# Kernel tuning notes

Measured on AMD Instinct MI355X. Metric: run time of the kernel, lower is better.

The kernel has to match this reference:

```python
import jax, jax.numpy as jnp
import numpy as np

HIDDEN = 512
NUM_EXPERTS = 8


def moe_top1(h, gate_w, We, be):
    # h: [B,S,d]; gate_w: [d,E]; We: [E,d,d]; be: [E,d]
    logits = jnp.einsum('bsd,de->bse', h, gate_w)
    probs = jax.nn.softmax(logits, axis=-1)            # [B,S,E]
    idx = jnp.argmax(probs, axis=-1)                   # [B,S] top-1 expert
    top_p = jnp.max(probs, axis=-1)                    # [B,S] gate weight
    # dense per-expert outputs then one-hot select (reference form of dispatch/combine)
    y_all = jnp.einsum('bsd,edf->bsef', h, We) + be    # [B,S,E,d]
    onehot = jax.nn.one_hot(idx, NUM_EXPERTS, dtype=h.dtype)
    out = jnp.einsum('bse,bsef->bsf', onehot, y_all)
    return out * top_p[..., None]


def setup_inputs() -> dict:
    key = jax.random.key(0)
    ks = jax.random.split(key, 10)
    B, S, d, E = 8, 2048, HIDDEN, NUM_EXPERTS
    s = 1.0 / np.sqrt(d)
    return {
        'x':   jax.random.normal(ks[0], (B, S, d), dtype=jnp.float32),
        'W1':  jax.random.uniform(ks[1], (d, d), jnp.float32, -s, s),
        'b1':  jax.random.uniform(ks[2], (d,), jnp.float32, -s, s),
        'gw2': jax.random.uniform(ks[3], (d, E), jnp.float32, -s, s),
        'We2': jax.random.uniform(ks[4], (E, d, d), jnp.float32, -s, s),
        'be2': jax.random.uniform(ks[5], (E, d), jnp.float32, -s, s),
        'gw3': jax.random.uniform(ks[6], (d, E), jnp.float32, -s, s),
        'We3': jax.random.uniform(ks[7], (E, d, d), jnp.float32, -s, s),
        'be3': jax.random.uniform(ks[8], (E, d), jnp.float32, -s, s),
        'y':   jax.random.randint(ks[9], (B,), 0, d, dtype=jnp.int64 if jax.config.jax_enable_x64 else jnp.int32),
    }


def reference(x, W1, b1, gw2, We2, be2, gw3, We3, be3, y):
    h = jnp.einsum('bsd,fd->bsf', x, W1.T.T @ jnp.eye(W1.shape[0], dtype=W1.dtype)) if False else x @ W1.T + b1  # Linear(d,d)
    out = moe_top1(h, gw2, We2, be2)
    out = moe_top1(out, gw3, We3, be3)
    hidden = h + out
    sentence_embed = hidden.mean(axis=1)               # [B, d]
    logp = jax.nn.log_softmax(sentence_embed, axis=-1)
    loss = -jnp.take_along_axis(logp, y[:, None].astype(jnp.int32), axis=1).mean()
    return loss
```

## Files before the change

kernel.cpp:

```cpp
#include <hip/hip_runtime.h>
#include <cstdint>

#define T_TOK 16384
#define D     512
#define E     8

typedef __attribute__((ext_vector_type(4))) float f32x4;
typedef __attribute__((ext_vector_type(8))) short short8v;
typedef __attribute__((ext_vector_type(8))) unsigned short u16x8;

__device__ __forceinline__ unsigned short f2bf(float f) {
    unsigned u = __float_as_uint(f);
    u += 0x7FFF + ((u >> 16) & 1);
    return (unsigned short)(u >> 16);
}
__device__ __forceinline__ float bf2f(unsigned short h) {
    return __uint_as_float((unsigned)h << 16);
}
__device__ __forceinline__ int swz(int r, int g) {
    return (r << 6) + (((g ^ ((r >> 1) & 3)) & 3) << 4);
}

__global__ __launch_bounds__(256) void k_conv_w1(const float* __restrict__ W,
                                                 unsigned short* __restrict__ hi,
                                                 unsigned short* __restrict__ lo,
                                                 int* __restrict__ c2,
                                                 int* __restrict__ c3,
                                                 float* __restrict__ embed)
{
    const int tid = threadIdx.x;
    if (blockIdx.x == 256) {
        if (tid < E) { c2[tid] = 0; c3[tid] = 0; }
        for (int i = tid; i < 8 * D; i += 256) embed[i] = 0.f;
        return;
    }
    const int i = (blockIdx.x * 256 + tid) * 4;
    const float4 v = *(const float4*)(W + i);
    const float f[4] = {v.x, v.y, v.z, v.w};
    unsigned short h[4], l[4];
#pragma unroll
    for (int j = 0; j < 4; ++j) {
        h[j] = f2bf(f[j]);
        l[j] = f2bf(f[j] - bf2f(h[j]));
    }
    *(uint2*)(hi + i) = *(uint2*)h;
    *(uint2*)(lo + i) = *(uint2*)l;
}

__global__ __launch_bounds__(256) void k_prep_we(const float* __restrict__ We2,
                                                 const float* __restrict__ We3,
                                                 unsigned short* __restrict__ hi2,
                                                 unsigned short* __restrict__ lo2,
                                                 unsigned short* __restrict__ hi3,
                                                 unsigned short* __restrict__ lo3)
{
    __shared__ float t[32][33];
    const int z = blockIdx.z;
    const int e = z & 7;
    const float* src = (z < 8 ? We2 : We3) + ((size_t)e << 18);
    unsigned short* dh = (z < 8 ? hi2 : hi3) + ((size_t)e << 18);
    unsigned short* dl = (z < 8 ? lo2 : lo3) + ((size_t)e << 18);
    const int k0 = blockIdx.x << 5, n0 = blockIdx.y << 5;
    const int tx = threadIdx.x & 31, ty = threadIdx.x >> 5;
#pragma unroll
    for (int i = 0; i < 32; i += 8)
        t[ty + i][tx] = src[(size_t)(k0 + ty + i) * D + n0 + tx];
    __syncthreads();
    const int n  = threadIdx.x >> 3;
    const int kc = (threadIdx.x & 7) << 2;
    unsigned short h4[4], l4[4];
#pragma unroll
    for (int j = 0; j < 4; ++j) {
        const float f = t[kc + j][n];
        h4[j] = f2bf(f);
        l4[j] = f2bf(f - bf2f(h4[j]));
    }
    const size_t o = (size_t)(n0 + n) * D + k0 + kc;
    *(uint2*)(dh + o) = *(uint2*)h4;
    *(uint2*)(dl + o) = *(uint2*)l4;
}

__global__ __launch_bounds__(256) void k_gating(const float* __restrict__ H,
                                                const float* __restrict__ gw,
                                                float* __restrict__ p,
                                                int* __restrict__ lists,
                                                int* __restrict__ counts)
{
    __shared__ float gws[D * E];
    __shared__ int histo[E], basex[E];
    const int tid = threadIdx.x;
    for (int i = tid; i < D * E; i += 256) gws[i] = gw[i];
    if (tid < E) histo[tid] = 0;
    __syncthreads();

    const int part = tid & 7;
    const int slot = tid >> 3;
    const int t0 = (blockIdx.x << 6) + slot;
    const int t1 = t0 + 32;
    const int d0 = part << 6;

    float a0[E], a1[E];
#pragma unroll
    for (int e = 0; e < E; ++e) { a0[e] = 0.f; a1[e] = 0.f; }
    const float* h0 = H + (size_t)t0 * D + d0;
    const float* h1 = H + (size_t)t1 * D + d0;
#pragma unroll 4
    for (int i = 0; i < 64; i += 4) {
        const float4 v0 = *(const float4*)(h0 + i);
        const float4 v1 = *(const float4*)(h1 + i);
        const float* gp = gws + (size_t)(d0 + i) * E;
#pragma unroll
        for (int j = 0; j < 4; ++j) {
            const f32x4 gA = *(const f32x4*)(gp + j * E);
            const f32x4 gB = *(const f32x4*)(gp + j * E + 4);
            const float x0 = (j == 0) ? v0.x : (j == 1) ? v0.y : (j == 2) ? v0.z : v0.w;
            const float x1 = (j == 0) ? v1.x : (j == 1) ? v1.y : (j == 2) ? v1.z : v1.w;
#pragma unroll
            for (int e = 0; e < 4; ++e) {
                a0[e]     += x0 * gA[e];
                a0[e + 4] += x0 * gB[e];
                a1[e]     += x1 * gA[e];
                a1[e + 4] += x1 * gB[e];
            }
        }
    }
#pragma unroll
    for (int e = 0; e < E; ++e) {
#pragma unroll
        for (int o = 1; o < 8; o <<= 1) {
            a0[e] += __shfl_xor(a0[e], o, 8);
            a1[e] += __shfl_xor(a1[e], o, 8);
        }
    }

    int mi0 = 0, mi1 = 0, r0 = 0, r1 = 0;
    if (part == 0) {
        float m0 = a0[0], m1 = a1[0];
#pragma unroll
        for (int e = 1; e < E; ++e) {
            if (a0[e] > m0) { m0 = a0[e]; mi0 = e; }
            if (a1[e] > m1) { m1 = a1[e]; mi1 = e; }
        }
        float s0 = 0.f, s1 = 0.f;
#pragma unroll
        for (int e = 0; e < E; ++e) { s0 += expf(a0[e] - m0); s1 += expf(a1[e] - m1); }
        p[t0] = 1.0f / s0;
        p[t1] = 1.0f / s1;
        r0 = atomicAdd(&histo[mi0], 1);
        r1 = atomicAdd(&histo[mi1], 1);
    }
    __syncthreads();
    if (tid < E) basex[tid] = atomicAdd(&counts[tid], histo[tid]);
    __syncthreads();
    if (part == 0) {
        lists[mi0 * T_TOK + basex[mi0] + r0] = t0;
        lists[mi1 * T_TOK + basex[mi1] + r1] = t1;
    }
}

template <bool GATHER>
__global__ __launch_bounds__(256, 2) void k_gemm_mfma(
    const float* __restrict__ A,
    const unsigned short* __restrict__ Bh,
    const unsigned short* __restrict__ Bl,
    const float* __restrict__ bias,
    const float* __restrict__ scale,
    const int* __restrict__ lists,
    const int* __restrict__ counts,
    float* __restrict__ C)
{
    __shared__ __align__(16) char sAh[8192];
    __shared__ __align__(16) char sAl[8192];
    __shared__ __align__(16) char sBh[8192];
    __shared__ __align__(16) char sBl[8192];
    __shared__ int Ts[128];

    const int tid = threadIdx.x;
    const int cpx = gridDim.x >> 3;
    const int wg  = (blockIdx.x & 7) * cpx + (blockIdx.x >> 3);
    const int mt  = wg >> 2;
    const int n0  = (wg & 3) << 7;

    int listoff = 0, mcnt = 128;
    size_t boff = 0;
    const float* bb = bias;
    if constexpr (GATHER) {
        int acc8 = 0, eSel = -1, mstart = 0;
#pragma unroll
        for (int i = 0; i < 8; ++i) {
            const int c = counts[i];
            const int nt = (c + 127) >> 7;
            if (eSel < 0 && mt < acc8 + nt) { eSel = i; mstart = (mt - acc8) << 7; }
            acc8 += nt;
        }
        if (eSel < 0) return;
        mcnt = min(128, counts[eSel] - mstart);
        listoff = eSel * T_TOK + mstart;
        boff = (size_t)eSel << 18;
        bb = bias + (eSel << 9);
    }

    if (tid < 128) {
        int t;
        if constexpr (GATHER) t = (tid < mcnt) ? lists[listoff + tid] : -1;
        else                  t = (mt << 7) + tid;
        Ts[tid] = t;
    }
    __syncthreads();

    const int srow = tid >> 1;
    const int sk   = (tid & 1) << 4;
    const int tA   = Ts[srow];
    const float* ap = A + (size_t)(tA < 0 ? 0 : tA) * D + sk;
    const unsigned short* bph = Bh + boff + (size_t)(n0 + srow) * D + sk;
    const unsigned short* bpl = Bl + boff + (size_t)(n0 + srow) * D + sk;
    const int g0  = sk >> 3;
    const int wa0 = swz(srow, g0), wa1 = swz(srow, g0 + 1);

    float4 av0 = *(const float4*)ap,        av1 = *(const float4*)(ap + 4),
           av2 = *(const float4*)(ap + 8),  av3 = *(const float4*)(ap + 12);
    uint4 bh0 = *(const uint4*)bph, bh1 = *(const uint4*)(bph + 8);
    uint4 bl0 = *(const uint4*)bpl, bl1 = *(const uint4*)(bpl + 8);

    const int wid = tid >> 6, lane = tid & 63;
    const int wr = (wid >> 1) << 6;
    const int wc = (wid & 1) << 6;
    const int fr = lane & 15;
    const int fg = lane >> 4;

    f32x4 acc[4][4] = {};

#pragma unroll 1
    for (int kt = 0; kt < 16; ++kt) {
        u16x8 h0, h1, l0, l1;
        {
            float f[16];
            *(float4*)&f[0] = av0; *(float4*)&f[4]  = av1;
            *(float4*)&f[8] = av2; *(float4*)&f[12] = av3;
#pragma unroll
            for (int i = 0; i < 8; ++i) {
                const unsigned short hh = f2bf(f[i]);
                h0[i] = hh;
                l0[i] = f2bf(f[i] - bf2f(hh));
            }
#pragma unroll
            for (int i = 0; i < 8; ++i) {
                const unsigned short hh = f2bf(f[8 + i]);
                h1[i] = hh;
                l1[i] = f2bf(f[8 + i] - bf2f(hh));
            }
        }
        __syncthreads();
        *(u16x8*)(sAh + wa0) = h0;  *(u16x8*)(sAh + wa1) = h1;
        *(u16x8*)(sAl + wa0) = l0;  *(u16x8*)(sAl + wa1) = l1;
        *(uint4*)(sBh + wa0) = bh0; *(uint4*)(sBh + wa1) = bh1;
        *(uint4*)(sBl + wa0) = bl0; *(uint4*)(sBl + wa1) = bl1;
        __syncthreads();
        if (kt < 15) {
            ap += 32; bph += 32; bpl += 32;
            av0 = *(const float4*)ap;       av1 = *(const float4*)(ap + 4);
            av2 = *(const float4*)(ap + 8); av3 = *(const float4*)(ap + 12);
            bh0 = *(const uint4*)bph; bh1 = *(const uint4*)(bph + 8);
            bl0 = *(const uint4*)bpl; bl1 = *(const uint4*)(bpl + 8);
        }

        short8v a_h[4], a_l[4], b_h[4], b_l[4];
#pragma unroll
        for (int i = 0; i < 4; ++i) {
            const int r = wr + i * 16 + fr;
            a_h[i] = *(const short8v*)(sAh + swz(r, fg));
            a_l[i] = *(const short8v*)(sAl + swz(r, fg));
        }
#pragma unroll
        for (int j = 0; j < 4; ++j) {
            const int r = wc + j * 16 + fr;
            b_h[j] = *(const short8v*)(sBh + swz(r, fg));
            b_l[j] = *(const short8v*)(sBl + swz(r, fg));
        }
#pragma unroll
        for (int i = 0; i < 4; ++i)
#pragma unroll
            for (int j = 0; j < 4; ++j) {
                acc[i][j] = __builtin_amdgcn_mfma_f32_16x16x32_bf16(a_h[i], b_h[j], acc[i][j], 0, 0, 0);
                acc[i][j] = __builtin_amdgcn_mfma_f32_16x16x32_bf16(a_h[i], b_l[j], acc[i][j], 0, 0, 0);
                acc[i][j] = __builtin_amdgcn_mfma_f32_16x16x32_bf16(a_l[i], b_h[j], acc[i][j], 0, 0, 0);
            }
    }

    float bj[4];
#pragma unroll
    for (int j = 0; j < 4; ++j) bj[j] = bb[n0 + wc + j * 16 + fr];
#pragma unroll
    for (int i = 0; i < 4; ++i) {
#pragma unroll
        for (int r = 0; r < 4; ++r) {
            const int m = wr + i * 16 + fg * 4 + r;
            const int t = Ts[m];
            if (t < 0) continue;
            float s = 1.f;
            if constexpr (GATHER) s = scale[t];
            float* cp = C + (size_t)t * D + n0 + wc;
#pragma unroll
            for (int j = 0; j < 4; ++j)
                cp[j * 16 + fr] = (acc[i][j][r] + bj[j]) * s;
        }
    }
}

__global__ __launch_bounds__(256) void k_reduce(const float* __restrict__ H,
                                                const float* __restrict__ O3,
                                                float* __restrict__ embed)
{
    const int b = blockIdx.x;
    const int sc = blockIdx.y;
    const int f = threadIdx.x;
    const size_t base = ((size_t)b * 2048 + (size_t)sc * 32) * D;
    const float* hb = H + base;
    const float* ob = O3 + base;
    float a0 = 0.f, a1 = 0.f;
#pragma unroll 4
    for (int s = 0; s < 32; ++s) {
        a0 += hb[s * D + f]       + ob[s * D + f];
        a1 += hb[s * D + f + 256] + ob[s * D + f + 256];
    }
    atomicAdd(&embed[b * D + f],       a0 * (1.0f / 2048.0f));
    atomicAdd(&embed[b * D + f + 256], a1 * (1.0f / 2048.0f));
}

__global__ __launch_bounds__(512) void k_loss(const float* __restrict__ embed,
                                              const int* __restrict__ y,
                                              float* __restrict__ out)
{
    __shared__ float partial[8];
    const int w = threadIdx.x >> 6;
    const int lane = threadIdx.x & 63;
    const float* row = embed + w * D;

    float v[8];
    float vmax = -1e30f;
#pragma unroll
    for (int i = 0; i < 8; ++i) {
        v[i] = row[lane + i * 64];
        vmax = fmaxf(vmax, v[i]);
    }
#pragma unroll
    for (int o = 32; o > 0; o >>= 1) vmax = fmaxf(vmax, __shfl_xor(vmax, o));
    float s = 0.f;
#pragma unroll
    for (int i = 0; i < 8; ++i) s += expf(v[i] - vmax);
#pragma unroll
    for (int o = 32; o > 0; o >>= 1) s += __shfl_xor(s, o);
    const float lse = vmax + logf(s);
    if (lane == 0) partial[w] = lse - row[y[w]];
    __syncthreads();
    if (threadIdx.x == 0) {
        float l = 0.f;
#pragma unroll
        for (int b = 0; b < 8; ++b) l += partial[b];
        out[0] = l * (1.0f / 8.0f);
    }
}

extern "C" void kernel_launch(void* const* d_in, const int* in_sizes, int n_in,
                              void* d_out, int out_size, void* d_ws, size_t ws_size,
                              hipStream_t stream)
{
    const float* x   = (const float*)d_in[0];
    const float* W1  = (const float*)d_in[1];
    const float* b1  = (const float*)d_in[2];
    const float* gw2 = (const float*)d_in[3];
    const float* We2 = (const float*)d_in[4];
    const float* be2 = (const float*)d_in[5];
    const float* gw3 = (const float*)d_in[6];
    const float* We3 = (const float*)d_in[7];
    const float* be3 = (const float*)d_in[8];
    const int*   y   = (const int*)d_in[9];
    float* out = (float*)d_out;

    char* ws = (char*)d_ws;
    size_t off = 0;
    auto alloc = [&](size_t bytes) -> void* {
        void* p = ws + off;
        off = (off + bytes + 255) & ~(size_t)255;
        return p;
    };
    float* h     = (float*)alloc((size_t)T_TOK * D * 4);
    float* out2  = (float*)alloc((size_t)T_TOK * D * 4);
    float* out3  = (float*)alloc((size_t)T_TOK * D * 4);
    unsigned short* b1h  = (unsigned short*)alloc((size_t)D * D * 2);
    unsigned short* b1l  = (unsigned short*)alloc((size_t)D * D * 2);
    unsigned short* we2h = (unsigned short*)alloc((size_t)E * D * D * 2);
    unsigned short* we2l = (unsigned short*)alloc((size_t)E * D * D * 2);
    unsigned short* we3h = (unsigned short*)alloc((size_t)E * D * D * 2);
    unsigned short* we3l = (unsigned short*)alloc((size_t)E * D * D * 2);
    float* p2    = (float*)alloc((size_t)T_TOK * 4);
    float* p3    = (float*)alloc((size_t)T_TOK * 4);
    int*   l2    = (int*)alloc((size_t)E * T_TOK * 4);
    int*   l3    = (int*)alloc((size_t)E * T_TOK * 4);
    int*   c2    = (int*)alloc(E * 4);
    int*   c3    = (int*)alloc(E * 4);
    float* embed = (float*)alloc(8 * D * 4);
    (void)ws_size; (void)in_sizes; (void)n_in; (void)out_size;

    k_conv_w1<<<dim3(257), dim3(256), 0, stream>>>(W1, b1h, b1l, c2, c3, embed);
    k_prep_we<<<dim3(16, 16, 16), dim3(256), 0, stream>>>(We2, We3, we2h, we2l, we3h, we3l);

    k_gemm_mfma<false><<<dim3(512), dim3(256), 0, stream>>>(
        x, b1h, b1l, b1, nullptr, nullptr, nullptr, h);

    k_gating<<<dim3(256), dim3(256), 0, stream>>>(h, gw2, p2, l2, c2);
    k_gemm_mfma<true><<<dim3(544), dim3(256), 0, stream>>>(
        h, we2h, we2l, be2, p2, l2, c2, out2);

    k_gating<<<dim3(256), dim3(256), 0, stream>>>(out2, gw3, p3, l3, c3);
    k_gemm_mfma<true><<<dim3(544), dim3(256), 0, stream>>>(
        out2, we3h, we3l, be3, p3, l3, c3, out3);

    k_reduce<<<dim3(8, 64), dim3(256), 0, stream>>>(h, out3, embed);
    k_loss<<<dim3(1), dim3(512), 0, stream>>>(embed, y, out);
}
```

Before: 267.8 us.

## Pre-split activations to bf16 hi/lo and stream tiles via global_load_lds

Activations are now split into bf16 hi/lo pairs once: x by a new conversion kernel, and h and out2 inside the GEMM epilogue, which writes extra bf16 copies next to the fp32 output. The GEMM main loop no longer converts fp32 on the fly. It loads all four operand tiles straight from global memory into LDS with global_load_lds, so the register staging and conversion ALU work go away. The cost is extra global writes for the bf16 copies, and the prefetch overlap is lost, because each load is now issued between two barriers within the same iteration. The x copies reuse the out3 buffer, which is safe only because out3 is written later.

```diff
diff --git a/kernel.cpp b/kernel.cpp
--- a/kernel.cpp
+++ b/kernel.cpp
@@ -7,7 +7,6 @@
 
 typedef __attribute__((ext_vector_type(4))) float f32x4;
 typedef __attribute__((ext_vector_type(8))) short short8v;
-typedef __attribute__((ext_vector_type(8))) unsigned short u16x8;
 
 __device__ __forceinline__ unsigned short f2bf(float f) {
     unsigned u = __float_as_uint(f);
@@ -19,6 +18,11 @@
 }
 __device__ __forceinline__ int swz(int r, int g) {
     return (r << 6) + (((g ^ ((r >> 1) & 3)) & 3) << 4);
+}
+__device__ __forceinline__ void gload16(const void* g, void* s) {
+    __builtin_amdgcn_global_load_lds(
+        (const __attribute__((address_space(1))) unsigned int*)g,
+        (__attribute__((address_space(3))) unsigned int*)s, 16, 0, 0);
 }
 
 __global__ __launch_bounds__(256) void k_conv_w1(const float* __restrict__ W,
@@ -45,6 +49,27 @@
     }
     *(uint2*)(hi + i) = *(uint2*)h;
     *(uint2*)(lo + i) = *(uint2*)l;
+}
+
+__global__ __launch_bounds__(256) void k_conv_x(const float* __restrict__ x,
+                                                unsigned short* __restrict__ xh,
+                                                unsigned short* __restrict__ xl)
+{
+    const size_t i = ((size_t)blockIdx.x * 256 + threadIdx.x) * 16;
+    float f[16];
+#pragma unroll
+    for (int q = 0; q < 4; ++q)
+        *(float4*)&f[q * 4] = *(const float4*)(x + i + q * 4);
+    unsigned short h[16], l[16];
+#pragma unroll
+    for (int j = 0; j < 16; ++j) {
+        h[j] = f2bf(f[j]);
+        l[j] = f2bf(f[j] - bf2f(h[j]));
+    }
+    *(uint4*)(xh + i)     = *(uint4*)&h[0];
+    *(uint4*)(xh + i + 8) = *(uint4*)&h[8];
+    *(uint4*)(xl + i)     = *(uint4*)&l[0];
+    *(uint4*)(xl + i + 8) = *(uint4*)&l[8];
 }
 
 __global__ __launch_bounds__(256) void k_prep_we(const float* __restrict__ We2,
@@ -158,16 +183,19 @@
     }
 }
 
-template <bool GATHER>
+template <bool GATHER, bool OUTCONV>
 __global__ __launch_bounds__(256, 2) void k_gemm_mfma(
-    const float* __restrict__ A,
+    const unsigned short* __restrict__ Ah,
+    const unsigned short* __restrict__ Al,
     const unsigned short* __restrict__ Bh,
     const unsigned short* __restrict__ Bl,
     const float* __restrict__ bias,
     const float* __restrict__ scale,
     const int* __restrict__ lists,
     const int* __restrict__ counts,
-    float* __restrict__ C)
+    float* __restrict__ C,
+    unsigned short* __restrict__ Ch,
+    unsigned short* __restrict__ Cl)
 {
     __shared__ __align__(16) char sAh[8192];
     __shared__ __align__(16) char sAl[8192];
@@ -208,21 +236,28 @@
     }
     __syncthreads();
 
-    const int srow = tid >> 1;
-    const int sk   = (tid & 1) << 4;
-    const int tA   = Ts[srow];
-    const float* ap = A + (size_t)(tA < 0 ? 0 : tA) * D + sk;
-    const unsigned short* bph = Bh + boff + (size_t)(n0 + srow) * D + sk;
-    const unsigned short* bpl = Bl + boff + (size_t)(n0 + srow) * D + sk;
-    const int g0  = sk >> 3;
-    const int wa0 = swz(srow, g0), wa1 = swz(srow, g0 + 1);
-
-    float4 av0 = *(const float4*)ap,        av1 = *(const float4*)(ap + 4),
-           av2 = *(const float4*)(ap + 8),  av3 = *(const float4*)(ap + 12);
-    uint4 bh0 = *(const uint4*)bph, bh1 = *(const uint4*)(bph + 8);
-    uint4 bl0 = *(const uint4*)bpl, bl1 = *(const uint4*)(bpl + 8);
-
     const int wid = tid >> 6, lane = tid & 63;
+
+    const int dr  = lane >> 2;
+    const int gsl = lane & 3;
+    const int r0 = (wid << 5) + dr, r1 = r0 + 16;
+    const int gg0 = ((gsl ^ ((r0 >> 1) & 3)) & 3) << 4;
+    const int gg1 = ((gsl ^ ((r1 >> 1) & 3)) & 3) << 4;
+    const int tA0 = Ts[r0] < 0 ? 0 : Ts[r0];
+    const int tA1 = Ts[r1] < 0 ? 0 : Ts[r1];
+    const char* pah0 = (const char*)Ah + ((size_t)tA0 << 10) + gg0;
+    const char* pah1 = (const char*)Ah + ((size_t)tA1 << 10) + gg1;
+    const char* pal0 = (const char*)Al + ((size_t)tA0 << 10) + gg0;
+    const char* pal1 = (const char*)Al + ((size_t)tA1 << 10) + gg1;
+    const char* pbh0 = (const char*)(Bh + boff) + ((size_t)(n0 + r0) << 10) + gg0;
+    const char* pbh1 = (const char*)(Bh + boff) + ((size_t)(n0 + r1) << 10) + gg1;
+    const char* pbl0 = (const char*)(Bl + boff) + ((size_t)(n0 + r0) << 10) + gg0;
+    const char* pbl1 = (const char*)(Bl + boff) + ((size_t)(n0 + r1) << 10) + gg1;
+    char* const dA0 = sAh + (wid << 11); char* const dA1 = dA0 + 1024;
+    char* const dL0 = sAl + (wid << 11); char* const dL1 = dL0 + 1024;
+    char* const dB0 = sBh + (wid << 11); char* const dB1 = dB0 + 1024;
+    char* const dC0 = sBl + (wid << 11); char* const dC1 = dC0 + 1024;
+
     const int wr = (wid >> 1) << 6;
     const int wc = (wid & 1) << 6;
     const int fr = lane & 15;
@@ -232,37 +267,14 @@
 
 #pragma unroll 1
     for (int kt = 0; kt < 16; ++kt) {
-        u16x8 h0, h1, l0, l1;
-        {
-            float f[16];
-            *(float4*)&f[0] = av0; *(float4*)&f[4]  = av1;
-            *(float4*)&f[8] = av2; *(float4*)&f[12] = av3;
-#pragma unroll
-            for (int i = 0; i < 8; ++i) {
-                const unsigned short hh = f2bf(f[i]);
-                h0[i] = hh;
-                l0[i] = f2bf(f[i] - bf2f(hh));
-            }
-#pragma unroll
-            for (int i = 0; i < 8; ++i) {
-                const unsigned short hh = f2bf(f[8 + i]);
-                h1[i] = hh;
-                l1[i] = f2bf(f[8 + i] - bf2f(hh));
-            }
-        }
         __syncthreads();
-        *(u16x8*)(sAh + wa0) = h0;  *(u16x8*)(sAh + wa1) = h1;
-        *(u16x8*)(sAl + wa0) = l0;  *(u16x8*)(sAl + wa1) = l1;
-        *(uint4*)(sBh + wa0) = bh0; *(uint4*)(sBh + wa1) = bh1;
-        *(uint4*)(sBl + wa0) = bl0; *(uint4*)(sBl + wa1) = bl1;
+        gload16(pah0, dA0); gload16(pah1, dA1);
+        gload16(pal0, dL0); gload16(pal1, dL1);
+        gload16(pbh0, dB0); gload16(pbh1, dB1);
+        gload16(pbl0, dC0); gload16(pbl1, dC1);
+        pah0 += 64; pah1 += 64; pal0 += 64; pal1 += 64;
+        pbh0 += 64; pbh1 += 64; pbl0 += 64; pbl1 += 64;
         __syncthreads();
-        if (kt < 15) {
-            ap += 32; bph += 32; bpl += 32;
-            av0 = *(const float4*)ap;       av1 = *(const float4*)(ap + 4);
-            av2 = *(const float4*)(ap + 8); av3 = *(const float4*)(ap + 12);
-            bh0 = *(const uint4*)bph; bh1 = *(const uint4*)(bph + 8);
-            bl0 = *(const uint4*)bpl; bl1 = *(const uint4*)(bpl + 8);
-        }
 
         short8v a_h[4], a_l[4], b_h[4], b_l[4];
 #pragma unroll
@@ -299,10 +311,18 @@
             if (t < 0) continue;
             float s = 1.f;
             if constexpr (GATHER) s = scale[t];
-            float* cp = C + (size_t)t * D + n0 + wc;
-#pragma unroll
-            for (int j = 0; j < 4; ++j)
-                cp[j * 16 + fr] = (acc[i][j][r] + bj[j]) * s;
+            const size_t rowo = (size_t)t * D + n0 + wc;
+#pragma unroll
+            for (int j = 0; j < 4; ++j) {
+                const float v = (acc[i][j][r] + bj[j]) * s;
+                const size_t o = rowo + j * 16 + fr;
+                C[o] = v;
+                if constexpr (OUTCONV) {
+                    const unsigned short hv = f2bf(v);
+                    Ch[o] = hv;
+                    Cl[o] = f2bf(v - bf2f(hv));
+                }
+            }
         }
     }
 }
@@ -387,6 +407,12 @@
     float* h     = (float*)alloc((size_t)T_TOK * D * 4);
     float* out2  = (float*)alloc((size_t)T_TOK * D * 4);
     float* out3  = (float*)alloc((size_t)T_TOK * D * 4);
+    unsigned short* xh = (unsigned short*)out3;
+    unsigned short* xl = xh + (size_t)T_TOK * D;
+    unsigned short* hh  = (unsigned short*)alloc((size_t)T_TOK * D * 2);
+    unsigned short* hl  = (unsigned short*)alloc((size_t)T_TOK * D * 2);
+    unsigned short* o2h = (unsigned short*)alloc((size_t)T_TOK * D * 2);
+    unsigned short* o2l = (unsigned short*)alloc((size_t)T_TOK * D * 2);
     unsigned short* b1h  = (unsigned short*)alloc((size_t)D * D * 2);
     unsigned short* b1l  = (unsigned short*)alloc((size_t)D * D * 2);
     unsigned short* we2h = (unsigned short*)alloc((size_t)E * D * D * 2);
@@ -404,17 +430,18 @@
 
     k_conv_w1<<<dim3(257), dim3(256), 0, stream>>>(W1, b1h, b1l, c2, c3, embed);
     k_prep_we<<<dim3(16, 16, 16), dim3(256), 0, stream>>>(We2, We3, we2h, we2l, we3h, we3l);
-
-    k_gemm_mfma<false><<<dim3(512), dim3(256), 0, stream>>>(
-        x, b1h, b1l, b1, nullptr, nullptr, nullptr, h);
+    k_conv_x<<<dim3(2048), dim3(256), 0, stream>>>(x, xh, xl);
+
+    k_gemm_mfma<false, true><<<dim3(512), dim3(256), 0, stream>>>(
+        xh, xl, b1h, b1l, b1, nullptr, nullptr, nullptr, h, hh, hl);
 
     k_gating<<<dim3(256), dim3(256), 0, stream>>>(h, gw2, p2, l2, c2);
-    k_gemm_mfma<true><<<dim3(544), dim3(256), 0, stream>>>(
-        h, we2h, we2l, be2, p2, l2, c2, out2);
+    k_gemm_mfma<true, true><<<dim3(544), dim3(256), 0, stream>>>(
+        hh, hl, we2h, we2l, be2, p2, l2, c2, out2, o2h, o2l);
 
     k_gating<<<dim3(256), dim3(256), 0, stream>>>(out2, gw3, p3, l3, c3);
-    k_gemm_mfma<true><<<dim3(544), dim3(256), 0, stream>>>(
-        out2, we3h, we3l, be3, p3, l3, c3, out3);
+    k_gemm_mfma<true, false><<<dim3(544), dim3(256), 0, stream>>>(
+        o2h, o2l, we3h, we3l, be3, p3, l3, c3, out3, nullptr, nullptr);
 
     k_reduce<<<dim3(8, 64), dim3(256), 0, stream>>>(h, out3, embed);
     k_loss<<<dim3(1), dim3(512), 0, stream>>>(embed, y, out);
```

New measurement: 281.3 us. +5.1%, slower.
